# Performance work log

Hardware: AMD Instinct MI355X
Metric: run time of the kernel (lower is better)

## Reference

```python
import jax, jax.numpy as jnp
import numpy as np

D_MODEL = 1024
HEADS = 16
D_K = D_MODEL // HEADS
B, S = 2, 2048


def setup_inputs() -> dict:
    key = jax.random.key(0)
    ks = jax.random.split(key, 11)
    sc = 1.0 / np.sqrt(D_MODEL)
    inp = {
        "q": jax.random.normal(ks[0], (B, S, D_MODEL), jnp.float32),
        "k": jax.random.normal(ks[1], (B, S, D_MODEL), jnp.float32),
        "v": jax.random.normal(ks[2], (B, S, D_MODEL), jnp.float32),
        # causal mask, broadcastable to (B, H, S, S); 0 -> masked
        "mask": jnp.tril(jnp.ones((S, S), jnp.int32))[None, None],
        "w_q": jax.random.normal(ks[3], (D_MODEL, D_MODEL), jnp.float32) * sc,
        "b_q": jax.random.normal(ks[4], (D_MODEL,), jnp.float32) * sc,
        "w_k": jax.random.normal(ks[5], (D_MODEL, D_MODEL), jnp.float32) * sc,
        "b_k": jax.random.normal(ks[6], (D_MODEL,), jnp.float32) * sc,
        "w_v": jax.random.normal(ks[7], (D_MODEL, D_MODEL), jnp.float32) * sc,
        "b_v": jax.random.normal(ks[8], (D_MODEL,), jnp.float32) * sc,
        "w_o": jax.random.normal(ks[9], (D_MODEL, D_MODEL), jnp.float32) * sc,
        "b_o": jax.random.normal(ks[10], (D_MODEL,), jnp.float32) * sc,
    }
    return inp


def reference(q, k, v, mask, w_q, b_q, w_k, b_k, w_v, b_v, w_o, b_o):
    b = q.shape[0]
    # torch Linear: x @ W.T + b
    Q = q @ w_q.T + b_q
    K = k @ w_k.T + b_k
    V = v @ w_v.T + b_v
    # (B, S, D) -> (B, H, S, d_k)
    Q = Q.reshape(b, -1, HEADS, D_K).transpose(0, 2, 1, 3)
    K = K.reshape(b, -1, HEADS, D_K).transpose(0, 2, 1, 3)
    V = V.reshape(b, -1, HEADS, D_K).transpose(0, 2, 1, 3)
    scores = jnp.einsum("bhqd,bhkd->bhqk", Q, K) / np.sqrt(D_K).astype(np.float32)
    scores = jnp.where(mask == 0, -jnp.inf, scores)
    attn = jax.nn.softmax(scores, axis=-1)
    out = jnp.einsum("bhqk,bhkd->bhqd", attn, V)
    out = out.transpose(0, 2, 1, 3).reshape(b, -1, D_MODEL)
    # dropout is identity in eval mode
    return out @ w_o.T + b_o
```

## Files before the change

### kernel.cpp

```cpp
#include <hip/hip_runtime.h>
#include <math.h>

#define D_MODEL 1024
#define N_HEADS 16
#define DKH     64
#define BATCH   2
#define SEQ     2048
#define NT256   (SEQ/256)
#define PARTS_PER_BH 20

typedef unsigned short u16;
typedef unsigned long long u64;
typedef __attribute__((ext_vector_type(8))) short short8;
typedef __attribute__((ext_vector_type(4))) short s4v;
typedef __attribute__((ext_vector_type(4))) float f32x4;

__device__ __forceinline__ u16 f2bf(float f) {
    unsigned u = __float_as_uint(f);
    u += 0x7fffu + ((u >> 16) & 1u);
    return (u16)(u >> 16);
}
__device__ __forceinline__ float bf2f(u16 x) {
    return __int_as_float(((int)x) << 16);
}

__device__ __forceinline__ float fexp2(float x) {
#if __has_builtin(__builtin_amdgcn_exp2f)
    return __builtin_amdgcn_exp2f(x);
#else
    return exp2f(x);
#endif
}

__device__ __forceinline__ void gll16(const void* g, void* l) {
    __builtin_amdgcn_global_load_lds((const __attribute__((address_space(1))) void*)g,
                                     (__attribute__((address_space(3))) void*)l, 16, 0, 0);
}

__device__ __forceinline__ f32x4 mfma16(s4v a, s4v b, f32x4 c) {
#if __has_builtin(__builtin_amdgcn_mfma_f32_16x16x16bf16_1k)
    return __builtin_amdgcn_mfma_f32_16x16x16bf16_1k(a, b, c, 0, 0, 0);
#elif __has_builtin(__builtin_amdgcn_mfma_f32_16x16x16_bf16)
    return __builtin_amdgcn_mfma_f32_16x16x16_bf16(a, b, c, 0, 0, 0);
#else
    f32x4 d;
    asm("v_mfma_f32_16x16x16_bf16 %0, %1, %2, %3" : "=v"(d) : "v"(a), "v"(b), "v"(c));
    return d;
#endif
}

__device__ __forceinline__ int vperm(int d) {
    return ((d & 7) << 3) | (((d >> 3) & 1) << 2);
}

__global__ __launch_bounds__(256)
void convert_kernel(const float* __restrict__ q, const float* __restrict__ k,
                    const float* __restrict__ v, const float* __restrict__ wq,
                    const float* __restrict__ wk, const float* __restrict__ wv,
                    const float* __restrict__ wo,
                    u16* __restrict__ qb, u16* __restrict__ kb, u16* __restrict__ vb,
                    u16* __restrict__ wqb, u16* __restrict__ wkb,
                    u16* __restrict__ wvb, u16* __restrict__ wob)
{
    const size_t NV = ((size_t)16 << 20) >> 3;
    for (size_t i = (size_t)blockIdx.x * blockDim.x + threadIdx.x; i < NV;
         i += (size_t)gridDim.x * blockDim.x) {
        const size_t e = i << 3;
        const float* s; u16* d; size_t off;
        if (e < ((size_t)12 << 20)) {
            const int seg = (int)(e >> 22);
            off = e & (((size_t)1 << 22) - 1);
            s = seg == 0 ? q : seg == 1 ? k : v;
            d = seg == 0 ? qb : seg == 1 ? kb : vb;
        } else {
            const size_t r = e - ((size_t)12 << 20);
            const int seg = (int)(r >> 20);
            off = r & (((size_t)1 << 20) - 1);
            s = seg == 0 ? wq : seg == 1 ? wk : seg == 2 ? wv : wo;
            d = seg == 0 ? wqb : seg == 1 ? wkb : seg == 2 ? wvb : wob;
        }
        const float4 f0 = *(const float4*)(s + off);
        const float4 f1 = *(const float4*)(s + off + 4);
        short8 o;
        o[0]=(short)f2bf(f0.x); o[1]=(short)f2bf(f0.y); o[2]=(short)f2bf(f0.z); o[3]=(short)f2bf(f0.w);
        o[4]=(short)f2bf(f1.x); o[5]=(short)f2bf(f1.y); o[6]=(short)f2bf(f1.z); o[7]=(short)f2bf(f1.w);
        *(short8*)(d + off) = o;
    }
}

#define GEMM_PREAMBLE                                                            \
    __shared__ __align__(16) u16 As[2][128][32];                                 \
    __shared__ __align__(16) u16 Bs[2][128][32];                                 \
    const int tid  = threadIdx.x;                                                \
    const int lane = tid & 63;                                                   \
    const int wid  = tid >> 6;                                                   \
    const int wm   = wid >> 1, wn = wid & 1;                                     \
    const int lr   = lane & 15, lg = lane >> 4;                                  \
    const int mb   = blockIdx.x * 128, nb = blockIdx.y * 128;                    \
    const int g_row = lane >> 2;                                                 \
    const int g_col = (lane & 3) << 3;                                           \
    const u16* Ab = A  + (size_t)mb * K;                                         \
    const u16* Bb = Bw + (size_t)nb * K;                                         \
    f32x4 acc[4][4];                                                             \
    _Pragma("unroll")                                                            \
    for (int i = 0; i < 4; ++i)                                                  \
        _Pragma("unroll")                                                        \
        for (int j = 0; j < 4; ++j) { f32x4 z = {0.f,0.f,0.f,0.f}; acc[i][j] = z; }

#define STAGE(buf, kt)                                                           \
    {                                                                            \
        _Pragma("unroll")                                                        \
        for (int t = 0; t < 2; ++t) {                                            \
            const int r0 = t*64 + wid*16;                                        \
            gll16(&Ab[(size_t)(r0 + g_row)*K + (kt) + g_col], &As[buf][r0][0]);  \
            gll16(&Bb[(size_t)(r0 + g_row)*K + (kt) + g_col], &Bs[buf][r0][0]);  \
        }                                                                        \
    }

#define GEMM_MAINLOOP                                                            \
    STAGE(0, 0)                                                                  \
    __syncthreads();                                                             \
    const int NK = K >> 5;                                                       \
    for (int it = 0; it < NK; ++it) {                                            \
        const int c = it & 1;                                                    \
        if (it + 1 < NK) STAGE(c ^ 1, (it + 1) << 5)                             \
        short8 a[4], b[4];                                                       \
        _Pragma("unroll")                                                        \
        for (int i = 0; i < 4; ++i) a[i] = *(const short8*)&As[c][wm*64 + i*16 + lr][lg*8]; \
        _Pragma("unroll")                                                        \
        for (int j = 0; j < 4; ++j) b[j] = *(const short8*)&Bs[c][wn*64 + j*16 + lr][lg*8]; \
        _Pragma("unroll")                                                        \
        for (int i = 0; i < 4; ++i)                                              \
            _Pragma("unroll")                                                    \
            for (int j = 0; j < 4; ++j)                                          \
                acc[i][j] = __builtin_amdgcn_mfma_f32_16x16x32_bf16(a[i], b[j], acc[i][j], 0, 0, 0); \
        __syncthreads();                                                         \
    }

__global__ __launch_bounds__(256, 3)
void gemm_qkv_kernel(const u16* __restrict__ qb, const u16* __restrict__ kb,
                     const u16* __restrict__ vb, const u16* __restrict__ wqb,
                     const u16* __restrict__ wkb, const u16* __restrict__ wvb,
                     const float* __restrict__ b_q, const float* __restrict__ b_k,
                     const float* __restrict__ b_v,
                     u16* __restrict__ Qh, u16* __restrict__ Kh, u16* __restrict__ Vt,
                     int M, int N, int K)
{
    const int z = blockIdx.z;
    const u16* A    = z == 0 ? qb  : z == 1 ? kb  : vb;
    const u16* Bw   = z == 0 ? wqb : z == 1 ? wkb : wvb;
    const float* bias = z == 0 ? b_q : z == 1 ? b_k : b_v;
    u16* dst        = z == 0 ? Qh  : z == 1 ? Kh  : Vt;
    const float scale = z == 0 ? 0.18033688f : 1.0f;

    GEMM_PREAMBLE
    GEMM_MAINLOOP

    #pragma unroll
    for (int i = 0; i < 4; ++i) {
        #pragma unroll
        for (int j = 0; j < 4; ++j) {
            const int mbase = mb + wm*64 + i*16 + lg*4;
            const int n     = nb + wn*64 + j*16 + lr;
            const float bn  = bias[n];
            const int h = n >> 6, d = n & 63;
            #pragma unroll
            for (int r = 0; r < 4; ++r) {
                const int m = mbase + r;
                const int b = m >> 11, s = m & (SEQ - 1);
                const float val = (acc[i][j][r] + bn) * scale;
                if (z == 2) {
                    const int sp = (s & ~63) | ((s & 63) ^ vperm(d));
                    dst[(((size_t)(b*N_HEADS + h))*DKH + d)*SEQ + sp] = f2bf(val);
                } else {
                    dst[(((size_t)(b*N_HEADS + h))*SEQ + s)*DKH + d] = f2bf(val);
                }
            }
        }
    }
}

__global__ __launch_bounds__(256)
void gemm_out_kernel(const u16* __restrict__ A, const u16* __restrict__ Bw,
                     const float* __restrict__ bias, float* __restrict__ dst,
                     int M, int N, int K)
{
    __shared__ __align__(16) u16 As[2][128][32];
    __shared__ __align__(16) u16 Bs[2][64][32];

    const int tid  = threadIdx.x;
    const int lane = tid & 63;
    const int wid  = tid >> 6;
    const int wm   = wid >> 1, wn = wid & 1;
    const int lr   = lane & 15, lg = lane >> 4;
    const int mb   = blockIdx.x * 128, nb = blockIdx.y * 64;
    const int g_row = lane >> 2;
    const int g_col = (lane & 3) << 3;

    const u16* Ab = A  + (size_t)mb * K;
    const u16* Bb = Bw + (size_t)nb * K;

    f32x4 acc[4][2];
    #pragma unroll
    for (int i = 0; i < 4; ++i)
        #pragma unroll
        for (int j = 0; j < 2; ++j) { f32x4 z = {0.f,0.f,0.f,0.f}; acc[i][j] = z; }

#define OSTAGE(buf, kt)                                                          \
    {                                                                            \
        _Pragma("unroll")                                                        \
        for (int t = 0; t < 2; ++t) {                                            \
            const int r0 = t*64 + wid*16;                                        \
            gll16(&Ab[(size_t)(r0 + g_row)*K + (kt) + g_col], &As[buf][r0][0]);  \
        }                                                                        \
        gll16(&Bb[(size_t)(wid*16 + g_row)*K + (kt) + g_col], &Bs[buf][wid*16][0]); \
    }

    OSTAGE(0, 0)
    __syncthreads();

    const int NK = K >> 5;
    for (int it = 0; it < NK; ++it) {
        const int c = it & 1;
        if (it + 1 < NK) OSTAGE(c ^ 1, (it + 1) << 5)

        short8 a[4], b[2];
        #pragma unroll
        for (int i = 0; i < 4; ++i) a[i] = *(const short8*)&As[c][wm*64 + i*16 + lr][lg*8];
        #pragma unroll
        for (int j = 0; j < 2; ++j) b[j] = *(const short8*)&Bs[c][wn*32 + j*16 + lr][lg*8];
        #pragma unroll
        for (int i = 0; i < 4; ++i)
            #pragma unroll
            for (int j = 0; j < 2; ++j)
                acc[i][j] = __builtin_amdgcn_mfma_f32_16x16x32_bf16(a[i], b[j], acc[i][j], 0, 0, 0);

        __syncthreads();
    }
#undef OSTAGE

    #pragma unroll
    for (int i = 0; i < 4; ++i) {
        #pragma unroll
        for (int j = 0; j < 2; ++j) {
            const int mbase = mb + wm*64 + i*16 + lg*4;
            const int n     = nb + wn*32 + j*16 + lr;
            const float bn  = bias[n];
            #pragma unroll
            for (int r = 0; r < 4; ++r)
                dst[(size_t)(mbase + r) * N + n] = acc[i][j][r] + bn;
        }
    }
}

__device__ __forceinline__ void attn_step2(
    const short8& aq00, const short8& aq01,
    const short8& aq10, const short8& aq11,
    f32x4 (&o0)[4], f32x4 (&o1)[4],
    float& osum0, float& osum1, float& m0, float& m1,
    const u16 (*__restrict__ Kl)[64], const u16 (*__restrict__ Vl)[64],
    int kvb, int qbw0, int qbw1, int lr, int lg)
{
    const int ksw  = (lr & 7) << 3;
    const int pvsw = vperm(lr);
    f32x4 st0[4], st1[4];
    __builtin_amdgcn_s_setprio(1);
    #pragma unroll
    for (int c = 0; c < 4; ++c) {
        const int kr = c*16 + lr;
        short8 k0 = *(const short8*)&Kl[kr][( 0 + lg*8) ^ ksw];
        short8 k1 = *(const short8*)&Kl[kr][(32 + lg*8) ^ ksw];
        f32x4 z0 = {0.f,0.f,0.f,0.f}, z1 = {0.f,0.f,0.f,0.f};
        z0 = __builtin_amdgcn_mfma_f32_16x16x32_bf16(k0, aq00, z0, 0, 0, 0);
        z1 = __builtin_amdgcn_mfma_f32_16x16x32_bf16(k0, aq10, z1, 0, 0, 0);
        z0 = __builtin_amdgcn_mfma_f32_16x16x32_bf16(k1, aq01, z0, 0, 0, 0);
        z1 = __builtin_amdgcn_mfma_f32_16x16x32_bf16(k1, aq11, z1, 0, 0, 0);
        st0[c] = z0; st1[c] = z1;
    }
    __builtin_amdgcn_s_setprio(0);

    if (kvb + 63 > qbw0) {
        #pragma unroll
        for (int c = 0; c < 4; ++c)
            #pragma unroll
            for (int r = 0; r < 4; ++r)
                if (kvb + c*16 + lg*4 + r > qbw0 + lr) st0[c][r] = -INFINITY;
    }
    if (kvb + 63 > qbw1) {
        #pragma unroll
        for (int c = 0; c < 4; ++c)
            #pragma unroll
            for (int r = 0; r < 4; ++r)
                if (kvb + c*16 + lg*4 + r > qbw1 + lr) st1[c][r] = -INFINITY;
    }

    float tl0 = fmaxf(fmaxf(st0[0][0], st0[0][1]), fmaxf(st0[0][2], st0[0][3]));
    float tl1 = fmaxf(fmaxf(st1[0][0], st1[0][1]), fmaxf(st1[0][2], st1[0][3]));
    #pragma unroll
    for (int c = 1; c < 4; ++c) {
        tl0 = fmaxf(tl0, fmaxf(fmaxf(st0[c][0], st0[c][1]), fmaxf(st0[c][2], st0[c][3])));
        tl1 = fmaxf(tl1, fmaxf(fmaxf(st1[c][0], st1[c][1]), fmaxf(st1[c][2], st1[c][3])));
    }
    if (__any(tl0 > m0 + 11.5f)) {
        float tm = fmaxf(tl0, __shfl_xor(tl0, 16));
        tm = fmaxf(tm, __shfl_xor(tm, 32));
        const float mnew  = fmaxf(m0, tm);
        const float alpha = fexp2(m0 - mnew);
        m0 = mnew; osum0 *= alpha;
        float af[4];
        #pragma unroll
        for (int r = 0; r < 4; ++r)
            af[r] = __shfl(alpha, (lg << 4) | (lg*4 + r));
        #pragma unroll
        for (int db = 0; db < 4; ++db)
            #pragma unroll
            for (int r = 0; r < 4; ++r) o0[db][r] *= af[r];
    }
    if (__any(tl1 > m1 + 11.5f)) {
        float tm = fmaxf(tl1, __shfl_xor(tl1, 16));
        tm = fmaxf(tm, __shfl_xor(tm, 32));
        const float mnew  = fmaxf(m1, tm);
        const float alpha = fexp2(m1 - mnew);
        m1 = mnew; osum1 *= alpha;
        float af[4];
        #pragma unroll
        for (int r = 0; r < 4; ++r)
            af[r] = __shfl(alpha, (lg << 4) | (lg*4 + r));
        #pragma unroll
        for (int db = 0; db < 4; ++db)
            #pragma unroll
            for (int r = 0; r < 4; ++r) o1[db][r] *= af[r];
    }

    s4v av0[4], av1[4];
    float sum0 = 0.f, sum1 = 0.f;
    #pragma unroll
    for (int c = 0; c < 4; ++c) {
        const float p0 = fexp2(st0[c][0] - m0);
        const float p1 = fexp2(st0[c][1] - m0);
        const float p2 = fexp2(st0[c][2] - m0);
        const float p3 = fexp2(st0[c][3] - m0);
        sum0 += (p0 + p1) + (p2 + p3);
        unsigned lo, hi;
        asm("v_cvt_pk_bf16_f32 %0, %1, %2" : "=v"(lo) : "v"(p0), "v"(p1));
        asm("v_cvt_pk_bf16_f32 %0, %1, %2" : "=v"(hi) : "v"(p2), "v"(p3));
        union { unsigned u[2]; s4v s; } uu; uu.u[0] = lo; uu.u[1] = hi;
        av0[c] = uu.s;
    }
    #pragma unroll
    for (int c = 0; c < 4; ++c) {
        const float p0 = fexp2(st1[c][0] - m1);
        const float p1 = fexp2(st1[c][1] - m1);
        const float p2 = fexp2(st1[c][2] - m1);
        const float p3 = fexp2(st1[c][3] - m1);
        sum1 += (p0 + p1) + (p2 + p3);
        unsigned lo, hi;
        asm("v_cvt_pk_bf16_f32 %0, %1, %2" : "=v"(lo) : "v"(p0), "v"(p1));
        asm("v_cvt_pk_bf16_f32 %0, %1, %2" : "=v"(hi) : "v"(p2), "v"(p3));
        union { unsigned u[2]; s4v s; } uu; uu.u[0] = lo; uu.u[1] = hi;
        av1[c] = uu.s;
    }
    osum0 += sum0; osum1 += sum1;

    __builtin_amdgcn_s_setprio(1);
    #pragma unroll
    for (int c = 0; c < 4; ++c) {
        #pragma unroll
        for (int db = 0; db < 4; ++db) {
            union { u64 q; s4v s; } bv;
            bv.q = *(const u64*)&Vl[db*16 + lr][(c*16 + lg*4) ^ pvsw];
            o0[db] = mfma16(av0[c], bv.s, o0[db]);
            o1[db] = mfma16(av1[c], bv.s, o1[db]);
        }
    }
    __builtin_amdgcn_s_setprio(0);
}

__global__ __launch_bounds__(512)
void flash_split_kernel(const u16* __restrict__ Qh, const u16* __restrict__ Kh,
                        const u16* __restrict__ Vt, u16* __restrict__ part_o,
                        float* __restrict__ part_ms)
{
    __shared__ __align__(16) u16 Kl[2][64][64];
    __shared__ __align__(16) u16 Vl[2][64][64];

    const int x = 19 - blockIdx.x;
    int t2, ch;
    if      (x <  1) { t2 = 0; ch = 0;      }
    else if (x <  2) { t2 = 1; ch = 0;      }
    else if (x <  4) { t2 = 2; ch = x - 2;  }
    else if (x <  6) { t2 = 3; ch = x - 4;  }
    else if (x <  9) { t2 = 4; ch = x - 6;  }
    else if (x < 12) { t2 = 5; ch = x - 9;  }
    else if (x < 16) { t2 = 6; ch = x - 12; }
    else             { t2 = 7; ch = x - 16; }

    const int tid  = threadIdx.x;
    const int lane = tid & 63;
    const int wid  = tid >> 6;
    const int lr   = lane & 15, lg = lane >> 4;
    const int bh   = blockIdx.y;
    const int qbw0 = t2*256 + wid*32;
    const int qbw1 = qbw0 + 16;
    const size_t base = (size_t)bh * SEQ * DKH;

    const int c0      = ch * 8;
    const int nc_here = min(8, 4*(t2+1) - c0);

    const int srow8 = lane >> 3;
    const int srow  = wid*8 + srow8;
    const int kcol  = ((lane & 7) << 3) ^ (srow8 << 3);
    const int vcol  = (lane & 7) << 3;

#define FSTAGE(buf, kb)                                                          \
    {                                                                            \
        gll16(&Kh[base + (size_t)((kb) + srow)*DKH + kcol], &Kl[buf][wid*8][0]); \
        gll16(&Vt[base + (size_t)srow*SEQ + (kb) + vcol],  &Vl[buf][wid*8][0]);  \
    }

    short8 aq00 = *(const short8*)&Qh[base + (size_t)(qbw0 + lr)*DKH +  0 + lg*8];
    short8 aq01 = *(const short8*)&Qh[base + (size_t)(qbw0 + lr)*DKH + 32 + lg*8];
    short8 aq10 = *(const short8*)&Qh[base + (size_t)(qbw1 + lr)*DKH +  0 + lg*8];
    short8 aq11 = *(const short8*)&Qh[base + (size_t)(qbw1 + lr)*DKH + 32 + lg*8];

    f32x4 o0[4], o1[4];
    float osum0 = 0.f, osum1 = 0.f, m0 = -INFINITY, m1 = -INFINITY;
    {
        f32x4 z = {0.f,0.f,0.f,0.f};
        #pragma unroll
        for (int db = 0; db < 4; ++db) { o0[db] = z; o1[db] = z; }
    }

    FSTAGE(0, c0*64)
    __syncthreads();

    for (int ci = 0; ci < nc_here; ++ci) {
        const int p = ci & 1;
        if (ci + 1 < nc_here) FSTAGE(p ^ 1, (c0 + ci + 1)*64)

        const int kvb = (c0 + ci) * 64;
        if (kvb <= qbw1 + 15)
            attn_step2(aq00, aq01, aq10, aq11, o0, o1, osum0, osum1, m0, m1,
                       Kl[p], Vl[p], kvb, qbw0, qbw1, lr, lg);

        __syncthreads();
    }
#undef FSTAGE

    osum0 += __shfl_xor(osum0, 16);
    osum0 += __shfl_xor(osum0, 32);
    osum1 += __shfl_xor(osum1, 16);
    osum1 += __shfl_xor(osum1, 32);

    const size_t slot = (size_t)bh * PARTS_PER_BH + x;
    u16*   po = part_o  + (slot << 14);
    float* pm = part_ms + (slot << 9);
    #pragma unroll
    for (int db = 0; db < 4; ++db)
        #pragma unroll
        for (int r = 0; r < 4; ++r) {
            po[(wid*32      + lg*4 + r)*64 + db*16 + lr] = f2bf(o0[db][r]);
            po[(wid*32 + 16 + lg*4 + r)*64 + db*16 + lr] = f2bf(o1[db][r]);
        }
    if (lane < 16) {
        pm[(wid*32      + lane)*2 + 0] = m0;
        pm[(wid*32      + lane)*2 + 1] = osum0;
        pm[(wid*32 + 16 + lane)*2 + 0] = m1;
        pm[(wid*32 + 16 + lane)*2 + 1] = osum1;
    }
}

__global__ __launch_bounds__(512)
void merge_kernel(const u16* __restrict__ part_o, const float* __restrict__ part_ms,
                  u16* __restrict__ attb)
{
    const int t2  = blockIdx.x;
    const int bh  = blockIdx.y;
    const int nch = (t2 >> 1) + 1;
    const int bxt[8] = {0, 1, 2, 4, 6, 9, 12, 16};
    const int basex = bxt[t2];

    const int row = threadIdx.x >> 1;
    const int cb  = (threadIdx.x & 1) * 32;

    float mm[4], ss[4];
    float M = -INFINITY;
    for (int c = 0; c < nch; ++c) {
        const size_t slot = (size_t)bh * PARTS_PER_BH + basex + c;
        mm[c] = part_ms[(slot << 9) + row*2 + 0];
        ss[c] = part_ms[(slot << 9) + row*2 + 1];
        M = fmaxf(M, mm[c]);
    }
    float S = 0.f;
    float acc[32];
    #pragma unroll
    for (int j = 0; j < 32; ++j) acc[j] = 0.f;
    for (int c = 0; c < nch; ++c) {
        const float w = exp2f(mm[c] - M);
        S += w * ss[c];
        const size_t slot = (size_t)bh * PARTS_PER_BH + basex + c;
        const u16* po = part_o + (slot << 14) + row*64 + cb;
        #pragma unroll
        for (int g = 0; g < 4; ++g) {
            short8 v = *(const short8*)(po + g*8);
            #pragma unroll
            for (int j = 0; j < 8; ++j)
                acc[g*8 + j] += w * bf2f((u16)v[j]);
        }
    }
    const float inv = 1.f / S;
    const int b = bh >> 4, h = bh & 15;
    const int grow = t2*256 + row;
    u16* dst = attb + ((size_t)(b*SEQ + grow))*D_MODEL + h*64 + cb;
    #pragma unroll
    for (int g = 0; g < 4; ++g) {
        short8 ov;
        #pragma unroll
        for (int j = 0; j < 8; ++j) ov[j] = (short)f2bf(acc[g*8 + j] * inv);
        *(short8*)(dst + g*8) = ov;
    }
}

extern "C" void kernel_launch(void* const* d_in, const int* in_sizes, int n_in,
                              void* d_out, int out_size, void* d_ws, size_t ws_size,
                              hipStream_t stream)
{
    const float* q   = (const float*)d_in[0];
    const float* k   = (const float*)d_in[1];
    const float* v   = (const float*)d_in[2];
    const float* w_q = (const float*)d_in[4];
    const float* b_q = (const float*)d_in[5];
    const float* w_k = (const float*)d_in[6];
    const float* b_k = (const float*)d_in[7];
    const float* w_v = (const float*)d_in[8];
    const float* b_v = (const float*)d_in[9];
    const float* w_o = (const float*)d_in[10];
    const float* b_o = (const float*)d_in[11];

    char* ws = (char*)d_ws;
    const size_t MB = 1024*1024;
    u16* Qh   = (u16*)(ws +  0*MB);
    u16* Kh   = (u16*)(ws +  8*MB);
    u16* Vt   = (u16*)(ws + 16*MB);
    u16* qb   = (u16*)(ws + 24*MB);
    u16* kb   = (u16*)(ws + 32*MB);
    u16* vb   = (u16*)(ws + 40*MB);
    u16* wqb  = (u16*)(ws + 48*MB);
    u16* wkb  = (u16*)(ws + 50*MB);
    u16* wvb  = (u16*)(ws + 52*MB);
    u16* wob  = (u16*)(ws + 54*MB);
    u16* attb = qb;
    u16*   part_o  = (u16*)(ws + 32*MB);
    float* part_ms = (float*)(ws + 52*MB);

    const int M = BATCH * SEQ, N = D_MODEL, K = D_MODEL;

    convert_kernel<<<2048, 256, 0, stream>>>(q, k, v, w_q, w_k, w_v, w_o,
                                             qb, kb, vb, wqb, wkb, wvb, wob);
    gemm_qkv_kernel<<<dim3(M/128, N/128, 3), 256, 0, stream>>>(
        qb, kb, vb, wqb, wkb, wvb, b_q, b_k, b_v, Qh, Kh, Vt, M, N, K);
    flash_split_kernel<<<dim3(PARTS_PER_BH, BATCH*N_HEADS), 512, 0, stream>>>(
        Qh, Kh, Vt, part_o, part_ms);
    merge_kernel<<<dim3(NT256, BATCH*N_HEADS), 512, 0, stream>>>(part_o, part_ms, attb);
    gemm_out_kernel<<<dim3(M/128, N/64), 256, 0, stream>>>(attb, wob, b_o, (float*)d_out, M, N, K);
}
```

Measured before the change: 143.3 us.

## Shrink attention and output-GEMM tiles; fold max subtraction into MFMA accumulator

Attention work is split into 128-row query tiles with 256-thread blocks and 40 partial slots per head, doubling the grid so more blocks fill the CUs. The merge kernel is remapped to match. The output GEMM uses 64x64 tiles for a larger grid. The softmax now seeds the QK MFMA accumulator with the negated running max and performs the lazy rescale after PV, removing the per-step max reduction before exponentiation. This trades extra partial-merge traffic and smaller tiles with less reuse against better occupancy and shorter dependency chains.

```diff
diff --git a/kernel.cpp b/kernel.cpp
--- a/kernel.cpp
+++ b/kernel.cpp
@@ -6,8 +6,8 @@
 #define DKH     64
 #define BATCH   2
 #define SEQ     2048
-#define NT256   (SEQ/256)
-#define PARTS_PER_BH 20
+#define NT128   (SEQ/128)
+#define PARTS_PER_BH 40
 
 typedef unsigned short u16;
 typedef unsigned long long u64;
@@ -185,7 +185,7 @@
                      const float* __restrict__ bias, float* __restrict__ dst,
                      int M, int N, int K)
 {
-    __shared__ __align__(16) u16 As[2][128][32];
+    __shared__ __align__(16) u16 As[2][64][32];
     __shared__ __align__(16) u16 Bs[2][64][32];
 
     const int tid  = threadIdx.x;
@@ -193,26 +193,22 @@
     const int wid  = tid >> 6;
     const int wm   = wid >> 1, wn = wid & 1;
     const int lr   = lane & 15, lg = lane >> 4;
-    const int mb   = blockIdx.x * 128, nb = blockIdx.y * 64;
+    const int mb   = blockIdx.x * 64, nb = blockIdx.y * 64;
     const int g_row = lane >> 2;
     const int g_col = (lane & 3) << 3;
 
     const u16* Ab = A  + (size_t)mb * K;
     const u16* Bb = Bw + (size_t)nb * K;
 
-    f32x4 acc[4][2];
-    #pragma unroll
-    for (int i = 0; i < 4; ++i)
+    f32x4 acc[2][2];
+    #pragma unroll
+    for (int i = 0; i < 2; ++i)
         #pragma unroll
         for (int j = 0; j < 2; ++j) { f32x4 z = {0.f,0.f,0.f,0.f}; acc[i][j] = z; }
 
 #define OSTAGE(buf, kt)                                                          \
     {                                                                            \
-        _Pragma("unroll")                                                        \
-        for (int t = 0; t < 2; ++t) {                                            \
-            const int r0 = t*64 + wid*16;                                        \
-            gll16(&Ab[(size_t)(r0 + g_row)*K + (kt) + g_col], &As[buf][r0][0]);  \
-        }                                                                        \
+        gll16(&Ab[(size_t)(wid*16 + g_row)*K + (kt) + g_col], &As[buf][wid*16][0]); \
         gll16(&Bb[(size_t)(wid*16 + g_row)*K + (kt) + g_col], &Bs[buf][wid*16][0]); \
     }
 
@@ -224,13 +220,13 @@
         const int c = it & 1;
         if (it + 1 < NK) OSTAGE(c ^ 1, (it + 1) << 5)
 
-        short8 a[4], b[2];
-        #pragma unroll
-        for (int i = 0; i < 4; ++i) a[i] = *(const short8*)&As[c][wm*64 + i*16 + lr][lg*8];
+        short8 a[2], b[2];
+        #pragma unroll
+        for (int i = 0; i < 2; ++i) a[i] = *(const short8*)&As[c][wm*32 + i*16 + lr][lg*8];
         #pragma unroll
         for (int j = 0; j < 2; ++j) b[j] = *(const short8*)&Bs[c][wn*32 + j*16 + lr][lg*8];
         #pragma unroll
-        for (int i = 0; i < 4; ++i)
+        for (int i = 0; i < 2; ++i)
             #pragma unroll
             for (int j = 0; j < 2; ++j)
                 acc[i][j] = __builtin_amdgcn_mfma_f32_16x16x32_bf16(a[i], b[j], acc[i][j], 0, 0, 0);
@@ -240,10 +236,10 @@
 #undef OSTAGE
 
     #pragma unroll
-    for (int i = 0; i < 4; ++i) {
+    for (int i = 0; i < 2; ++i) {
         #pragma unroll
         for (int j = 0; j < 2; ++j) {
-            const int mbase = mb + wm*64 + i*16 + lg*4;
+            const int mbase = mb + wm*32 + i*16 + lg*4;
             const int n     = nb + wn*32 + j*16 + lr;
             const float bn  = bias[n];
             #pragma unroll
@@ -263,6 +259,7 @@
 {
     const int ksw  = (lr & 7) << 3;
     const int pvsw = vperm(lr);
+    const float nm0 = -m0, nm1 = -m1;
     f32x4 st0[4], st1[4];
     __builtin_amdgcn_s_setprio(1);
     #pragma unroll
@@ -270,7 +267,8 @@
         const int kr = c*16 + lr;
         short8 k0 = *(const short8*)&Kl[kr][( 0 + lg*8) ^ ksw];
         short8 k1 = *(const short8*)&Kl[kr][(32 + lg*8) ^ ksw];
-        f32x4 z0 = {0.f,0.f,0.f,0.f}, z1 = {0.f,0.f,0.f,0.f};
+        f32x4 z0 = {nm0, nm0, nm0, nm0};
+        f32x4 z1 = {nm1, nm1, nm1, nm1};
         z0 = __builtin_amdgcn_mfma_f32_16x16x32_bf16(k0, aq00, z0, 0, 0, 0);
         z1 = __builtin_amdgcn_mfma_f32_16x16x32_bf16(k0, aq10, z1, 0, 0, 0);
         z0 = __builtin_amdgcn_mfma_f32_16x16x32_bf16(k1, aq01, z0, 0, 0, 0);
@@ -294,53 +292,17 @@
                 if (kvb + c*16 + lg*4 + r > qbw1 + lr) st1[c][r] = -INFINITY;
     }
 
-    float tl0 = fmaxf(fmaxf(st0[0][0], st0[0][1]), fmaxf(st0[0][2], st0[0][3]));
-    float tl1 = fmaxf(fmaxf(st1[0][0], st1[0][1]), fmaxf(st1[0][2], st1[0][3]));
-    #pragma unroll
-    for (int c = 1; c < 4; ++c) {
-        tl0 = fmaxf(tl0, fmaxf(fmaxf(st0[c][0], st0[c][1]), fmaxf(st0[c][2], st0[c][3])));
-        tl1 = fmaxf(tl1, fmaxf(fmaxf(st1[c][0], st1[c][1]), fmaxf(st1[c][2], st1[c][3])));
-    }
-    if (__any(tl0 > m0 + 11.5f)) {
-        float tm = fmaxf(tl0, __shfl_xor(tl0, 16));
-        tm = fmaxf(tm, __shfl_xor(tm, 32));
-        const float mnew  = fmaxf(m0, tm);
-        const float alpha = fexp2(m0 - mnew);
-        m0 = mnew; osum0 *= alpha;
-        float af[4];
-        #pragma unroll
-        for (int r = 0; r < 4; ++r)
-            af[r] = __shfl(alpha, (lg << 4) | (lg*4 + r));
-        #pragma unroll
-        for (int db = 0; db < 4; ++db)
-            #pragma unroll
-            for (int r = 0; r < 4; ++r) o0[db][r] *= af[r];
-    }
-    if (__any(tl1 > m1 + 11.5f)) {
-        float tm = fmaxf(tl1, __shfl_xor(tl1, 16));
-        tm = fmaxf(tm, __shfl_xor(tm, 32));
-        const float mnew  = fmaxf(m1, tm);
-        const float alpha = fexp2(m1 - mnew);
-        m1 = mnew; osum1 *= alpha;
-        float af[4];
-        #pragma unroll
-        for (int r = 0; r < 4; ++r)
-            af[r] = __shfl(alpha, (lg << 4) | (lg*4 + r));
-        #pragma unroll
-        for (int db = 0; db < 4; ++db)
-            #pragma unroll
-            for (int r = 0; r < 4; ++r) o1[db][r] *= af[r];
-    }
-
     s4v av0[4], av1[4];
     float sum0 = 0.f, sum1 = 0.f;
+    float tl0 = -INFINITY, tl1 = -INFINITY;
     #pragma unroll
     for (int c = 0; c < 4; ++c) {
-        const float p0 = fexp2(st0[c][0] - m0);
-        const float p1 = fexp2(st0[c][1] - m0);
-        const float p2 = fexp2(st0[c][2] - m0);
-        const float p3 = fexp2(st0[c][3] - m0);
+        const float p0 = fexp2(st0[c][0]);
+        const float p1 = fexp2(st0[c][1]);
+        const float p2 = fexp2(st0[c][2]);
+        const float p3 = fexp2(st0[c][3]);
         sum0 += (p0 + p1) + (p2 + p3);
+        tl0 = fmaxf(tl0, fmaxf(fmaxf(st0[c][0], st0[c][1]), fmaxf(st0[c][2], st0[c][3])));
         unsigned lo, hi;
         asm("v_cvt_pk_bf16_f32 %0, %1, %2" : "=v"(lo) : "v"(p0), "v"(p1));
         asm("v_cvt_pk_bf16_f32 %0, %1, %2" : "=v"(hi) : "v"(p2), "v"(p3));
@@ -349,11 +311,12 @@
     }
     #pragma unroll
     for (int c = 0; c < 4; ++c) {
-        const float p0 = fexp2(st1[c][0] - m1);
-        const float p1 = fexp2(st1[c][1] - m1);
-        const float p2 = fexp2(st1[c][2] - m1);
-        const float p3 = fexp2(st1[c][3] - m1);
+        const float p0 = fexp2(st1[c][0]);
+        const float p1 = fexp2(st1[c][1]);
+        const float p2 = fexp2(st1[c][2]);
+        const float p3 = fexp2(st1[c][3]);
         sum1 += (p0 + p1) + (p2 + p3);
+        tl1 = fmaxf(tl1, fmaxf(fmaxf(st1[c][0], st1[c][1]), fmaxf(st1[c][2], st1[c][3])));
         unsigned lo, hi;
         asm("v_cvt_pk_bf16_f32 %0, %1, %2" : "=v"(lo) : "v"(p0), "v"(p1));
         asm("v_cvt_pk_bf16_f32 %0, %1, %2" : "=v"(hi) : "v"(p2), "v"(p3));
@@ -374,9 +337,40 @@
         }
     }
     __builtin_amdgcn_s_setprio(0);
-}
-
-__global__ __launch_bounds__(512)
+
+    if (__any(tl0 > 11.5f)) {
+        float tm = fmaxf(tl0, __shfl_xor(tl0, 16));
+        tm = fmaxf(tm, __shfl_xor(tm, 32));
+        tm = fmaxf(tm, 0.f);
+        const float f = fexp2(-tm);
+        m0 += tm; osum0 *= f;
+        float af[4];
+        #pragma unroll
+        for (int r = 0; r < 4; ++r)
+            af[r] = __shfl(f, (lg << 4) | (lg*4 + r));
+        #pragma unroll
+        for (int db = 0; db < 4; ++db)
+            #pragma unroll
+            for (int r = 0; r < 4; ++r) o0[db][r] *= af[r];
+    }
+    if (__any(tl1 > 11.5f)) {
+        float tm = fmaxf(tl1, __shfl_xor(tl1, 16));
+        tm = fmaxf(tm, __shfl_xor(tm, 32));
+        tm = fmaxf(tm, 0.f);
+        const float f = fexp2(-tm);
+        m1 += tm; osum1 *= f;
+        float af[4];
+        #pragma unroll
+        for (int r = 0; r < 4; ++r)
+            af[r] = __shfl(f, (lg << 4) | (lg*4 + r));
+        #pragma unroll
+        for (int db = 0; db < 4; ++db)
+            #pragma unroll
+            for (int r = 0; r < 4; ++r) o1[db][r] *= af[r];
+    }
+}
+
+__global__ __launch_bounds__(256)
 void flash_split_kernel(const u16* __restrict__ Qh, const u16* __restrict__ Kh,
                         const u16* __restrict__ Vt, u16* __restrict__ part_o,
                         float* __restrict__ part_ms)
@@ -384,38 +378,36 @@
     __shared__ __align__(16) u16 Kl[2][64][64];
     __shared__ __align__(16) u16 Vl[2][64][64];
 
-    const int x = 19 - blockIdx.x;
-    int t2, ch;
-    if      (x <  1) { t2 = 0; ch = 0;      }
-    else if (x <  2) { t2 = 1; ch = 0;      }
-    else if (x <  4) { t2 = 2; ch = x - 2;  }
-    else if (x <  6) { t2 = 3; ch = x - 4;  }
-    else if (x <  9) { t2 = 4; ch = x - 6;  }
-    else if (x < 12) { t2 = 5; ch = x - 9;  }
-    else if (x < 16) { t2 = 6; ch = x - 12; }
-    else             { t2 = 7; ch = x - 16; }
+    const int x = 39 - blockIdx.x;
+    int t, ch;
+    if      (x <  4) { t = x;                 ch = 0;        }
+    else if (x < 12) { t = 4 + ((x-4) >> 1);  ch = (x-4)&1;  }
+    else if (x < 24) { t = 8 + (x-12)/3;      ch = (x-12)%3; }
+    else             { t = 12 + ((x-24) >> 2); ch = (x-24)&3; }
 
     const int tid  = threadIdx.x;
     const int lane = tid & 63;
     const int wid  = tid >> 6;
     const int lr   = lane & 15, lg = lane >> 4;
     const int bh   = blockIdx.y;
-    const int qbw0 = t2*256 + wid*32;
+    const int qbw0 = t*128 + wid*32;
     const int qbw1 = qbw0 + 16;
     const size_t base = (size_t)bh * SEQ * DKH;
 
     const int c0      = ch * 8;
-    const int nc_here = min(8, 4*(t2+1) - c0);
+    const int nc_here = min(8, 2*(t+1) - c0);
 
     const int srow8 = lane >> 3;
-    const int srow  = wid*8 + srow8;
     const int kcol  = ((lane & 7) << 3) ^ (srow8 << 3);
     const int vcol  = (lane & 7) << 3;
+    const int sr0   = wid*16 + srow8;
 
 #define FSTAGE(buf, kb)                                                          \
     {                                                                            \
-        gll16(&Kh[base + (size_t)((kb) + srow)*DKH + kcol], &Kl[buf][wid*8][0]); \
-        gll16(&Vt[base + (size_t)srow*SEQ + (kb) + vcol],  &Vl[buf][wid*8][0]);  \
+        gll16(&Kh[base + (size_t)((kb) + sr0    )*DKH + kcol], &Kl[buf][wid*16    ][0]); \
+        gll16(&Kh[base + (size_t)((kb) + sr0 + 8)*DKH + kcol], &Kl[buf][wid*16 + 8][0]); \
+        gll16(&Vt[base + (size_t)(sr0    )*SEQ + (kb) + vcol], &Vl[buf][wid*16    ][0]); \
+        gll16(&Vt[base + (size_t)(sr0 + 8)*SEQ + (kb) + vcol], &Vl[buf][wid*16 + 8][0]); \
     }
 
     short8 aq00 = *(const short8*)&Qh[base + (size_t)(qbw0 + lr)*DKH +  0 + lg*8];
@@ -424,7 +416,7 @@
     short8 aq11 = *(const short8*)&Qh[base + (size_t)(qbw1 + lr)*DKH + 32 + lg*8];
 
     f32x4 o0[4], o1[4];
-    float osum0 = 0.f, osum1 = 0.f, m0 = -INFINITY, m1 = -INFINITY;
+    float osum0 = 0.f, osum1 = 0.f, m0 = 0.f, m1 = 0.f;
     {
         f32x4 z = {0.f,0.f,0.f,0.f};
         #pragma unroll
@@ -453,8 +445,8 @@
     osum1 += __shfl_xor(osum1, 32);
 
     const size_t slot = (size_t)bh * PARTS_PER_BH + x;
-    u16*   po = part_o  + (slot << 14);
-    float* pm = part_ms + (slot << 9);
+    u16*   po = part_o  + (slot << 13);
+    float* pm = part_ms + (slot << 8);
     #pragma unroll
     for (int db = 0; db < 4; ++db)
         #pragma unroll
@@ -470,15 +462,14 @@
     }
 }
 
-__global__ __launch_bounds__(512)
+__global__ __launch_bounds__(256)
 void merge_kernel(const u16* __restrict__ part_o, const float* __restrict__ part_ms,
                   u16* __restrict__ attb)
 {
-    const int t2  = blockIdx.x;
+    const int t   = blockIdx.x;
     const int bh  = blockIdx.y;
-    const int nch = (t2 >> 1) + 1;
-    const int bxt[8] = {0, 1, 2, 4, 6, 9, 12, 16};
-    const int basex = bxt[t2];
+    const int nch = min(4, (2*(t+1) + 7) >> 3);
+    const int basex = t < 4 ? t : t < 8 ? 4 + 2*(t-4) : t < 12 ? 12 + 3*(t-8) : 24 + 4*(t-12);
 
     const int row = threadIdx.x >> 1;
     const int cb  = (threadIdx.x & 1) * 32;
@@ -487,8 +478,8 @@
     float M = -INFINITY;
     for (int c = 0; c < nch; ++c) {
         const size_t slot = (size_t)bh * PARTS_PER_BH + basex + c;
-        mm[c] = part_ms[(slot << 9) + row*2 + 0];
-        ss[c] = part_ms[(slot << 9) + row*2 + 1];
+        mm[c] = part_ms[(slot << 8) + row*2 + 0];
+        ss[c] = part_ms[(slot << 8) + row*2 + 1];
         M = fmaxf(M, mm[c]);
     }
     float S = 0.f;
@@ -499,7 +490,7 @@
         const float w = exp2f(mm[c] - M);
         S += w * ss[c];
         const size_t slot = (size_t)bh * PARTS_PER_BH + basex + c;
-        const u16* po = part_o + (slot << 14) + row*64 + cb;
+        const u16* po = part_o + (slot << 13) + row*64 + cb;
         #pragma unroll
         for (int g = 0; g < 4; ++g) {
             short8 v = *(const short8*)(po + g*8);
@@ -510,7 +501,7 @@
     }
     const float inv = 1.f / S;
     const int b = bh >> 4, h = bh & 15;
-    const int grow = t2*256 + row;
+    const int grow = t*128 + row;
     u16* dst = attb + ((size_t)(b*SEQ + grow))*D_MODEL + h*64 + cb;
     #pragma unroll
     for (int g = 0; g < 4; ++g) {
@@ -559,8 +550,8 @@
                                              qb, kb, vb, wqb, wkb, wvb, wob);
     gemm_qkv_kernel<<<dim3(M/128, N/128, 3), 256, 0, stream>>>(
         qb, kb, vb, wqb, wkb, wvb, b_q, b_k, b_v, Qh, Kh, Vt, M, N, K);
-    flash_split_kernel<<<dim3(PARTS_PER_BH, BATCH*N_HEADS), 512, 0, stream>>>(
+    flash_split_kernel<<<dim3(PARTS_PER_BH, BATCH*N_HEADS), 256, 0, stream>>>(
         Qh, Kh, Vt, part_o, part_ms);
-    merge_kernel<<<dim3(NT256, BATCH*N_HEADS), 512, 0, stream>>>(part_o, part_ms, attb);
-    gemm_out_kernel<<<dim3(M/128, N/64), 256, 0, stream>>>(attb, wob, b_o, (float*)d_out, M, N, K);
-}
+    merge_kernel<<<dim3(NT128, BATCH*N_HEADS), 256, 0, stream>>>(part_o, part_ms, attb);
+    gemm_out_kernel<<<dim3(M/64, N/64), 256, 0, stream>>>(attb, wob, b_o, (float*)d_out, M, N, K);
+}
```

Result: faster. 136.2 us (-5.0%).
